# Kernel tuning notes

Hardware: AMD Instinct MI355X
Metric: run time of the kernel (lower is better)

The kernel has to match this reference:

```python
import jax, jax.numpy as jnp
import numpy as np

B, S, E = 4, 2048, 2048
H = 16
DH = 2048 // H  # head dim = 128


def setup_inputs() -> dict:
    key = jax.random.key(0)
    k0, k1, k2, k3 = jax.random.split(key, 4)
    scale = 1.0 / np.sqrt(E)
    embedded = jax.random.normal(k0, (B, S, E), dtype=jnp.float32)
    # stacked per-head projection weights, bias-free Linear: y = x @ W^T -> store as [H, E, DH]
    Wq = jax.random.normal(k1, (H, E, DH), dtype=jnp.float32) * scale
    Wk = jax.random.normal(k2, (H, E, DH), dtype=jnp.float32) * scale
    Wv = jax.random.normal(k3, (H, E, DH), dtype=jnp.float32) * scale
    return {"embedded": embedded, "Wq": Wq, "Wk": Wk, "Wv": Wv}


def reference(embedded, Wq, Wk, Wv):
    # batched over heads instead of the original python loop (same math)
    q = jnp.einsum("bse,hed->bhsd", embedded, Wq)
    k = jnp.einsum("bse,hed->bhsd", embedded, Wk)
    v = jnp.einsum("bse,hed->bhsd", embedded, Wv)
    scores = jnp.einsum("bhsd,bhtd->bhst", q, k) / jnp.sqrt(jnp.float32(DH))
    causal = jnp.tril(jnp.ones((S, S), dtype=bool))  # [S, S]
    scores = jnp.where(causal, scores, -jnp.inf)
    probs = jax.nn.softmax(scores, axis=-1)
    out = jnp.einsum("bhst,bhtd->bhsd", probs, v)
    cated = out.transpose(0, 2, 1, 3).reshape(B, S, H * DH)  # concat heads on dim=2
    return jnp.round(cated, 4)
```

## Files before the change

kernel.cpp:

```cpp
#include <hip/hip_runtime.h>

typedef float   f32x4 __attribute__((ext_vector_type(4)));
typedef _Float16 half8 __attribute__((ext_vector_type(8)));
typedef _Float16 half4 __attribute__((ext_vector_type(4)));

#define B_  4
#define S_  2048
#define E_  2048
#define H_  16
#define DH_ 128

__device__ __forceinline__ void gld16(const void* g, void* l) {
  __builtin_amdgcn_global_load_lds((const void __attribute__((address_space(1)))*)g,
                                   (void __attribute__((address_space(3)))*)l, 16, 0, 0);
}

__global__ __launch_bounds__(256) void k_cvt(const float* __restrict__ in,
                                             _Float16* __restrict__ out) {
  size_t i = ((size_t)blockIdx.x * 256 + threadIdx.x) * 8;
  float4 a = *(const float4*)(in + i);
  float4 b = *(const float4*)(in + i + 4);
  half8 h;
  h[0]=(_Float16)a.x; h[1]=(_Float16)a.y; h[2]=(_Float16)a.z; h[3]=(_Float16)a.w;
  h[4]=(_Float16)b.x; h[5]=(_Float16)b.y; h[6]=(_Float16)b.z; h[7]=(_Float16)b.w;
  *(half8*)(out + i) = h;
}

__global__ __launch_bounds__(256) void k_wt(const float* __restrict__ Wq, const float* __restrict__ Wk,
                                            const float* __restrict__ Wv, _Float16* __restrict__ Wqt,
                                            _Float16* __restrict__ Wkt, _Float16* __restrict__ Wvt) {
  __shared__ float t[32][33];
  int p = blockIdx.z >> 4, h = blockIdx.z & 15;
  const float* W  = (p==0) ? Wq  : (p==1) ? Wk  : Wv;
  _Float16*    Wt = (p==0) ? Wqt : (p==1) ? Wkt : Wvt;
  int e0 = blockIdx.x * 32, d0 = blockIdx.y * 32;
  int tx = threadIdx.x, ty = threadIdx.y;
  for (int i=0;i<4;i++)
    t[ty+8*i][tx] = W[((size_t)h*E_ + (e0+ty+8*i))*DH_ + d0+tx];
  __syncthreads();
  for (int i=0;i<4;i++)
    Wt[((size_t)h*DH_ + (d0+ty+8*i))*E_ + e0+tx] = (_Float16)t[tx][ty+8*i];
}

#define NT 32

__global__ __launch_bounds__(512, 2) void k_gemm(const _Float16* __restrict__ X,
    const _Float16* __restrict__ Wq, const _Float16* __restrict__ Wk, const _Float16* __restrict__ Wv,
    _Float16* __restrict__ Qo, _Float16* __restrict__ Ko, _Float16* __restrict__ Vt)
{
  __shared__ __align__(16) _Float16 pool[65536];

  const int z = blockIdx.z;
  const _Float16* Wp = (z==0) ? Wq : (z==1) ? Wk : Wv;

  const int fi  = blockIdx.x + (blockIdx.y << 5);
  const int lbx = fi >> 3, lby = fi & 7;
  const int m0 = lbx << 8, n0 = lby << 8;

  const int tid = threadIdx.x;
  const int wid = tid >> 6, lane = tid & 63, quad = lane >> 4, lcol = lane & 15;
  const int wm = wid >> 2, wn = wid & 3;

  int soff[2]; int slds[2];
  #pragma unroll
  for (int r=0;r<2;r++){
    int chunk = wid*128 + r*64 + lane;
    int row = chunk >> 3, cl = chunk & 7, cg = cl ^ (row & 7);
    soff[r] = row*E_ + cg*8;
    slds[r] = (wid*128 + r*64) * 16;
  }

  const _Float16* Ag = X  + (size_t)m0 * E_;
  const _Float16* Bg = Wp + (size_t)n0 * E_;

  auto stageA = [&](int mh, int tt, int buf){
    const _Float16* s = Ag + mh*(128*E_) + tt*64;
    char* l = (char*)pool + (buf*4096 + mh*1024)*16;
    #pragma unroll
    for (int r=0;r<2;r++) gld16(s + soff[r], l + slds[r]);
  };
  auto stageB = [&](int nh, int tt, int buf){
    const _Float16* s = Bg + nh*(128*E_) + tt*64;
    char* l = (char*)pool + (buf*4096 + (2+nh)*1024)*16;
    #pragma unroll
    for (int r=0;r<2;r++) gld16(s + soff[r], l + slds[r]);
  };

  half8 a[2][4], b[2][2];
  f32x4 acc[2][2][4][2] = {};

  auto rdA = [&](int mh, int buf){
    const _Float16* base = pool + (buf*4096 + mh*1024)*8;
    #pragma unroll
    for (int kk=0;kk<2;kk++)
      #pragma unroll
      for (int mi=0;mi<4;mi++){
        int R = wm*64 + mi*16 + lcol;
        int c = (kk*4 + quad) ^ (R & 7);
        a[kk][mi] = *(const half8*)(base + R*64 + c*8);
      }
  };
  auto rdB = [&](int nh, int buf){
    const _Float16* base = pool + (buf*4096 + (2+nh)*1024)*8;
    #pragma unroll
    for (int kk=0;kk<2;kk++)
      #pragma unroll
      for (int ni=0;ni<2;ni++){
        int R = wn*32 + ni*16 + lcol;
        int c = (kk*4 + quad) ^ (R & 7);
        b[kk][ni] = *(const half8*)(base + R*64 + c*8);
      }
  };
  auto mm = [&](f32x4 (&ac)[4][2]){
    #pragma unroll
    for (int kk=0;kk<2;kk++)
      #pragma unroll
      for (int mi=0;mi<4;mi++)
        #pragma unroll
        for (int ni=0;ni<2;ni++)
          ac[mi][ni] = __builtin_amdgcn_mfma_f32_16x16x32_f16(a[kk][mi], b[kk][ni], ac[mi][ni], 0, 0, 0);
  };

  stageA(0,0,0); stageB(0,0,0); stageA(1,0,0); stageB(1,0,0);
  stageA(0,1,1); stageB(1,1,1); stageA(1,1,1);
  asm volatile("s_waitcnt vmcnt(6)" ::: "memory");
  __builtin_amdgcn_s_barrier();

#define MFMA_OPEN() do{ __builtin_amdgcn_s_barrier(); \
    asm volatile("s_waitcnt lgkmcnt(0)" ::: "memory"); \
    __builtin_amdgcn_sched_barrier(0); \
    __builtin_amdgcn_s_setprio(1); }while(0)
#define MFMA_CLOSE() do{ __builtin_amdgcn_s_setprio(0); \
    __builtin_amdgcn_s_barrier(); }while(0)

#define TILE(T, BUF) do{ \
    rdA(0, BUF); rdB(0, BUF); \
    if ((T)+1 < NT) stageB(0, (T)+1, (BUF)^1); \
    MFMA_OPEN(); mm(acc[0][0]); MFMA_CLOSE(); \
    rdB(1, BUF); \
    if ((T)+2 < NT) stageA(0, (T)+2, BUF); \
    MFMA_OPEN(); mm(acc[0][1]); MFMA_CLOSE(); \
    rdA(1, BUF); \
    if ((T)+2 < NT) stageB(1, (T)+2, BUF); \
    MFMA_OPEN(); mm(acc[1][1]); MFMA_CLOSE(); \
    rdB(0, BUF); \
    if ((T)+2 < NT) stageA(1, (T)+2, BUF); \
    __builtin_amdgcn_s_barrier(); \
    asm volatile("s_waitcnt lgkmcnt(0)" ::: "memory"); \
    __builtin_amdgcn_sched_barrier(0); \
    __builtin_amdgcn_s_setprio(1); \
    mm(acc[1][0]); \
    __builtin_amdgcn_s_setprio(0); \
    if ((T) < NT-2)       { asm volatile("s_waitcnt vmcnt(6)" ::: "memory"); } \
    else if ((T) == NT-2) { asm volatile("s_waitcnt vmcnt(0)" ::: "memory"); } \
    __builtin_amdgcn_s_barrier(); \
  }while(0)

  for (int t = 0; t < NT; t += 2){
    TILE(t,   0);
    TILE(t+1, 1);
  }
#undef TILE
#undef MFMA_OPEN
#undef MFMA_CLOSE

  const int bb = m0 >> 11;
  const int s0 = m0 & 2047;
  const int h0 = n0 >> 7;
  if (z < 2){
    _Float16* O = z ? Ko : Qo;
    #pragma unroll
    for (int mh=0; mh<2; mh++)
      #pragma unroll
      for (int nh=0; nh<2; nh++)
        #pragma unroll
        for (int mi=0; mi<4; mi++)
          #pragma unroll
          for (int ni=0; ni<2; ni++){
            const int srow = s0 + mh*128 + wm*64 + mi*16 + quad*4;
            const int d = wn*32 + ni*16 + lcol;
            _Float16* p = O + (((size_t)bb*H_ + (h0+nh))*S_ + srow)*DH_ + d;
            const f32x4 v = acc[mh][nh][mi][ni];
            p[0]=(_Float16)v[0]; p[DH_]=(_Float16)v[1]; p[2*DH_]=(_Float16)v[2]; p[3*DH_]=(_Float16)v[3];
          }
  } else {
    #pragma unroll
    for (int mh=0; mh<2; mh++)
      #pragma unroll
      for (int nh=0; nh<2; nh++)
        #pragma unroll
        for (int mi=0; mi<4; mi++)
          #pragma unroll
          for (int ni=0; ni<2; ni++){
            const int scol = s0 + mh*128 + wm*64 + mi*16 + quad*4;
            const int d = wn*32 + ni*16 + lcol;
            const f32x4 u = acc[mh][nh][mi][ni];
            half4 v;
            v[0]=(_Float16)u[0]; v[1]=(_Float16)u[1]; v[2]=(_Float16)u[2]; v[3]=(_Float16)u[3];
            *(half4*)(Vt + (((size_t)bb*H_ + (h0+nh))*DH_ + d)*S_ + scol) = v;
          }
  }
}

__global__ __launch_bounds__(512, 2) void k_attn(const _Float16* __restrict__ Q,
    const _Float16* __restrict__ K, const _Float16* __restrict__ Vt, float* __restrict__ out)
{
  __shared__ __align__(16) _Float16 Ks[2][8192], Vs[2][8192];

  const int b = blockIdx.z, h = blockIdx.y;
  const int q0 = (gridDim.x - 1 - blockIdx.x) * 256;
  const int tid = threadIdx.x, wid = tid >> 6, lane = tid & 63, quad = lane >> 4, lcol = lane & 15;
  const size_t bh = (size_t)b*H_ + h;
  const _Float16* Qg = Q  + (bh*S_ + q0)*DH_;
  const _Float16* Kg = K  + bh*S_*DH_;
  const _Float16* Vg = Vt + bh*DH_*S_;

  int krow[2], kcg[2], vdr[2], vcg[2];
  for (int r=0;r<2;r++){
    int chunk = wid*128 + r*64 + lane;
    krow[r] = chunk >> 4;
    kcg[r]  = (chunk & 15) ^ (krow[r] & 15);
    vdr[r]  = chunk >> 3;
    vcg[r]  = (chunk & 7) ^ (vdr[r] & 7);
  }

  half8 qf[2][4];
  for (int g=0; g<2; g++)
    for (int kk=0; kk<4; kk++)
      qf[g][kk] = *(const half8*)(Qg + (size_t)(wid*32 + g*16 + lcol)*DH_ + kk*32 + quad*8);

  for (int r=0;r<2;r++){
    gld16(Kg + (size_t)krow[r]*DH_ + kcg[r]*8, (char*)Ks[0] + wid*2048 + r*1024 + lane*16);
    gld16(Vg + (size_t)vdr[r]*S_ + 0 + vcg[r]*8, (char*)Vs[0] + wid*2048 + r*1024 + lane*16);
  }

  f32x4 oaccT[2][8] = {};
  f32x4 lacc[2] = {};
  const half4 ones = {(_Float16)1.f,(_Float16)1.f,(_Float16)1.f,(_Float16)1.f};
  const float c1 = 0.12751879526654326f;
  const float c2 = -11.541560327111707f;
  const int rbase = q0 + wid*32;
  const int nt = (q0 >> 6) + 4;

  for (int t = 0; t < nt; t++) {
    const int buf = t & 1;
    const _Float16* ksb = Ks[buf];
    const _Float16* vsb = Vs[buf];
    const int j0 = t << 6;
    const bool live0 = (j0 <= rbase + 15);
    const bool live1 = (j0 <= rbase + 31);
    __syncthreads();

    f32x4 sa[2][4] = {};
    if (live0){
      for (int kk=0; kk<4; kk++){
        int cl = (kk*4 + quad) ^ lcol;
        for (int jb=0; jb<4; jb++){
          half8 kf = *(const half8*)(ksb + (size_t)(jb*16 + lcol)*DH_ + cl*8);
          sa[0][jb] = __builtin_amdgcn_mfma_f32_16x16x32_f16(kf, qf[0][kk], sa[0][jb], 0, 0, 0);
          sa[1][jb] = __builtin_amdgcn_mfma_f32_16x16x32_f16(kf, qf[1][kk], sa[1][jb], 0, 0, 0);
        }
      }
    } else if (live1){
      for (int kk=0; kk<4; kk++){
        int cl = (kk*4 + quad) ^ lcol;
        for (int jb=0; jb<4; jb++){
          half8 kf = *(const half8*)(ksb + (size_t)(jb*16 + lcol)*DH_ + cl*8);
          sa[1][jb] = __builtin_amdgcn_mfma_f32_16x16x32_f16(kf, qf[1][kk], sa[1][jb], 0, 0, 0);
        }
      }
    }

    if (t+1 < nt){
      const int j1 = (t+1) << 6;
      for (int r=0;r<2;r++){
        gld16(Kg + (size_t)(j1+krow[r])*DH_ + kcg[r]*8, (char*)Ks[buf^1] + wid*2048 + r*1024 + lane*16);
        gld16(Vg + (size_t)vdr[r]*S_ + j1 + vcg[r]*8,   (char*)Vs[buf^1] + wid*2048 + r*1024 + lane*16);
      }
    }

    if (live1){
      half4 pb[2][4];
      auto sm = [&](f32x4 (&s4)[4], half4 (&p4)[4], int rb){
        if (j0 + 63 > rb){
          for (int jb=0; jb<4; jb++)
            for (int rg=0; rg<4; rg++){
              int j = jb*16 + quad*4 + rg;
              float p = (j0 + j > rb + lcol) ? 0.f
                      : __builtin_amdgcn_exp2f(fmaf(s4[jb][rg], c1, c2));
              p4[jb][rg] = (_Float16)p;
            }
        } else {
          for (int jb=0; jb<4; jb++)
            for (int rg=0; rg<4; rg++)
              p4[jb][rg] = (_Float16)__builtin_amdgcn_exp2f(fmaf(s4[jb][rg], c1, c2));
        }
      };

      if (live0){
        sm(sa[0], pb[0], rbase);
        sm(sa[1], pb[1], rbase + 16);
        for (int jb=0; jb<4; jb++){
          lacc[0] = __builtin_amdgcn_mfma_f32_16x16x16f16(ones, pb[0][jb], lacc[0], 0, 0, 0);
          lacc[1] = __builtin_amdgcn_mfma_f32_16x16x16f16(ones, pb[1][jb], lacc[1], 0, 0, 0);
        }
        for (int dblk=0; dblk<8; dblk++){
          const _Float16* vrow = vsb + (size_t)(dblk*16 + lcol)*64;
          for (int jb=0; jb<4; jb++){
            int cl = (2*jb + (quad>>1)) ^ (lcol & 7);
            half4 va = *(const half4*)(vrow + cl*8 + (quad&1)*4);
            oaccT[0][dblk] = __builtin_amdgcn_mfma_f32_16x16x16f16(va, pb[0][jb], oaccT[0][dblk], 0, 0, 0);
            oaccT[1][dblk] = __builtin_amdgcn_mfma_f32_16x16x16f16(va, pb[1][jb], oaccT[1][dblk], 0, 0, 0);
          }
        }
      } else {
        sm(sa[1], pb[1], rbase + 16);
        for (int jb=0; jb<4; jb++)
          lacc[1] = __builtin_amdgcn_mfma_f32_16x16x16f16(ones, pb[1][jb], lacc[1], 0, 0, 0);
        for (int dblk=0; dblk<8; dblk++){
          const _Float16* vrow = vsb + (size_t)(dblk*16 + lcol)*64;
          for (int jb=0; jb<4; jb++){
            int cl = (2*jb + (quad>>1)) ^ (lcol & 7);
            half4 va = *(const half4*)(vrow + cl*8 + (quad&1)*4);
            oaccT[1][dblk] = __builtin_amdgcn_mfma_f32_16x16x16f16(va, pb[1][jb], oaccT[1][dblk], 0, 0, 0);
          }
        }
      }
    }
  }

  for (int g=0; g<2; g++){
    const float rinv = 1.f / lacc[g][0];
    const int s = q0 + wid*32 + g*16 + lcol;
    float* op = out + ((size_t)b*S_ + s)*(H_*DH_) + h*DH_ + quad*4;
    for (int dblk=0; dblk<8; dblk++){
      float4 v;
      v.x = oaccT[g][dblk][0]*rinv; v.y = oaccT[g][dblk][1]*rinv;
      v.z = oaccT[g][dblk][2]*rinv; v.w = oaccT[g][dblk][3]*rinv;
      *(float4*)(op + dblk*16) = v;
    }
  }
}

extern "C" void kernel_launch(void* const* d_in, const int* in_sizes, int n_in,
                              void* d_out, int out_size, void* d_ws, size_t ws_size,
                              hipStream_t stream) {
  const float* X  = (const float*)d_in[0];
  const float* Wq = (const float*)d_in[1];
  const float* Wk = (const float*)d_in[2];
  const float* Wv = (const float*)d_in[3];
  float* out = (float*)d_out;

  _Float16* Xh  = (_Float16*)d_ws;
  _Float16* Wqt = Xh  + (size_t)B_*S_*E_;
  _Float16* Wkt = Wqt + (size_t)H_*E_*DH_;
  _Float16* Wvt = Wkt + (size_t)H_*E_*DH_;
  _Float16* Qh  = Wvt + (size_t)H_*E_*DH_;
  _Float16* Kh  = Qh  + (size_t)B_*H_*S_*DH_;
  _Float16* Vth = Kh  + (size_t)B_*H_*S_*DH_;

  k_cvt <<<8192, 256, 0, stream>>>(X, Xh);
  k_wt  <<<dim3(E_/32, DH_/32, 3*H_), dim3(32,8), 0, stream>>>(Wq, Wk, Wv, Wqt, Wkt, Wvt);
  k_gemm<<<dim3(32, 8, 3), 512, 0, stream>>>(Xh, Wqt, Wkt, Wvt, Qh, Kh, Vth);
  k_attn<<<dim3(S_/256, H_, B_), 512, 0, stream>>>(Qh, Kh, Vth, out);
}
```

Measured before the change: 493.5 us.

## Double attention KV tile to 128 keys and remap GEMM blocks per XCD

```diff
diff --git a/kernel.cpp b/kernel.cpp
--- a/kernel.cpp
+++ b/kernel.cpp
@@ -54,7 +54,9 @@
   const _Float16* Wp = (z==0) ? Wq : (z==1) ? Wk : Wv;
 
   const int fi  = blockIdx.x + (blockIdx.y << 5);
-  const int lbx = fi >> 3, lby = fi & 7;
+  const int xcd = fi & 7, kk_ = fi >> 3;
+  const int lbx = ((xcd >> 1) << 3) | (kk_ & 7);
+  const int lby = ((xcd & 1) << 2) | (kk_ >> 3);
   const int m0 = lbx << 8, n0 = lby << 8;
 
   const int tid = threadIdx.x;
@@ -205,7 +207,7 @@
 __global__ __launch_bounds__(512, 2) void k_attn(const _Float16* __restrict__ Q,
     const _Float16* __restrict__ K, const _Float16* __restrict__ Vt, float* __restrict__ out)
 {
-  __shared__ __align__(16) _Float16 Ks[2][8192], Vs[2][8192];
+  __shared__ __align__(16) _Float16 Ks[2][16384], Vs[2][16384];
 
   const int b = blockIdx.z, h = blockIdx.y;
   const int q0 = (gridDim.x - 1 - blockIdx.x) * 256;
@@ -215,13 +217,11 @@
   const _Float16* Kg = K  + bh*S_*DH_;
   const _Float16* Vg = Vt + bh*DH_*S_;
 
-  int krow[2], kcg[2], vdr[2], vcg[2];
-  for (int r=0;r<2;r++){
-    int chunk = wid*128 + r*64 + lane;
-    krow[r] = chunk >> 4;
-    kcg[r]  = (chunk & 15) ^ (krow[r] & 15);
-    vdr[r]  = chunk >> 3;
-    vcg[r]  = (chunk & 7) ^ (vdr[r] & 7);
+  int srow[4], scg[4];
+  for (int r=0;r<4;r++){
+    int chunk = wid*256 + r*64 + lane;
+    srow[r] = chunk >> 4;
+    scg[r]  = (chunk & 15) ^ (srow[r] & 15);
   }
 
   half8 qf[2][4];
@@ -229,9 +229,9 @@
     for (int kk=0; kk<4; kk++)
       qf[g][kk] = *(const half8*)(Qg + (size_t)(wid*32 + g*16 + lcol)*DH_ + kk*32 + quad*8);
 
-  for (int r=0;r<2;r++){
-    gld16(Kg + (size_t)krow[r]*DH_ + kcg[r]*8, (char*)Ks[0] + wid*2048 + r*1024 + lane*16);
-    gld16(Vg + (size_t)vdr[r]*S_ + 0 + vcg[r]*8, (char*)Vs[0] + wid*2048 + r*1024 + lane*16);
+  for (int r=0;r<4;r++){
+    gld16(Kg + (size_t)srow[r]*DH_ + scg[r]*8, (char*)Ks[0] + wid*4096 + r*1024 + lane*16);
+    gld16(Vg + (size_t)srow[r]*S_  + scg[r]*8, (char*)Vs[0] + wid*4096 + r*1024 + lane*16);
   }
 
   f32x4 oaccT[2][8] = {};
@@ -240,46 +240,49 @@
   const float c1 = 0.12751879526654326f;
   const float c2 = -11.541560327111707f;
   const int rbase = q0 + wid*32;
-  const int nt = (q0 >> 6) + 4;
+  const int nt = (q0 >> 7) + 2;
 
   for (int t = 0; t < nt; t++) {
     const int buf = t & 1;
-    const _Float16* ksb = Ks[buf];
-    const _Float16* vsb = Vs[buf];
-    const int j0 = t << 6;
-    const bool live0 = (j0 <= rbase + 15);
-    const bool live1 = (j0 <= rbase + 31);
     __syncthreads();
 
-    f32x4 sa[2][4] = {};
-    if (live0){
-      for (int kk=0; kk<4; kk++){
-        int cl = (kk*4 + quad) ^ lcol;
-        for (int jb=0; jb<4; jb++){
-          half8 kf = *(const half8*)(ksb + (size_t)(jb*16 + lcol)*DH_ + cl*8);
-          sa[0][jb] = __builtin_amdgcn_mfma_f32_16x16x32_f16(kf, qf[0][kk], sa[0][jb], 0, 0, 0);
-          sa[1][jb] = __builtin_amdgcn_mfma_f32_16x16x32_f16(kf, qf[1][kk], sa[1][jb], 0, 0, 0);
-        }
-      }
-    } else if (live1){
-      for (int kk=0; kk<4; kk++){
-        int cl = (kk*4 + quad) ^ lcol;
-        for (int jb=0; jb<4; jb++){
-          half8 kf = *(const half8*)(ksb + (size_t)(jb*16 + lcol)*DH_ + cl*8);
-          sa[1][jb] = __builtin_amdgcn_mfma_f32_16x16x32_f16(kf, qf[1][kk], sa[1][jb], 0, 0, 0);
-        }
+    if (t+1 < nt){
+      const int j1 = (t+1) << 7;
+      for (int r=0;r<4;r++){
+        gld16(Kg + (size_t)(j1+srow[r])*DH_ + scg[r]*8, (char*)Ks[buf^1] + wid*4096 + r*1024 + lane*16);
+        gld16(Vg + (size_t)srow[r]*S_ + j1 + scg[r]*8,  (char*)Vs[buf^1] + wid*4096 + r*1024 + lane*16);
       }
     }
 
-    if (t+1 < nt){
-      const int j1 = (t+1) << 6;
-      for (int r=0;r<2;r++){
-        gld16(Kg + (size_t)(j1+krow[r])*DH_ + kcg[r]*8, (char*)Ks[buf^1] + wid*2048 + r*1024 + lane*16);
-        gld16(Vg + (size_t)vdr[r]*S_ + j1 + vcg[r]*8,   (char*)Vs[buf^1] + wid*2048 + r*1024 + lane*16);
-      }
-    }
-
-    if (live1){
+    #pragma unroll
+    for (int u=0; u<2; u++){
+      const int j0 = (t << 7) + (u << 6);
+      const _Float16* ksb = Ks[buf] + (u << 6)*128;
+      const _Float16* vsb = Vs[buf];
+      const bool live0 = (j0 <= rbase + 15);
+      const bool live1 = (j0 <= rbase + 31);
+      if (!live1) continue;
+
+      f32x4 sa[2][4] = {};
+      if (live0){
+        for (int kk=0; kk<4; kk++){
+          int cl = (kk*4 + quad) ^ lcol;
+          for (int jb=0; jb<4; jb++){
+            half8 kf = *(const half8*)(ksb + (size_t)(jb*16 + lcol)*128 + cl*8);
+            sa[0][jb] = __builtin_amdgcn_mfma_f32_16x16x32_f16(kf, qf[0][kk], sa[0][jb], 0, 0, 0);
+            sa[1][jb] = __builtin_amdgcn_mfma_f32_16x16x32_f16(kf, qf[1][kk], sa[1][jb], 0, 0, 0);
+          }
+        }
+      } else {
+        for (int kk=0; kk<4; kk++){
+          int cl = (kk*4 + quad) ^ lcol;
+          for (int jb=0; jb<4; jb++){
+            half8 kf = *(const half8*)(ksb + (size_t)(jb*16 + lcol)*128 + cl*8);
+            sa[1][jb] = __builtin_amdgcn_mfma_f32_16x16x32_f16(kf, qf[1][kk], sa[1][jb], 0, 0, 0);
+          }
+        }
+      }
+
       half4 pb[2][4];
       auto sm = [&](f32x4 (&s4)[4], half4 (&p4)[4], int rb){
         if (j0 + 63 > rb){
@@ -305,9 +308,9 @@
           lacc[1] = __builtin_amdgcn_mfma_f32_16x16x16f16(ones, pb[1][jb], lacc[1], 0, 0, 0);
         }
         for (int dblk=0; dblk<8; dblk++){
-          const _Float16* vrow = vsb + (size_t)(dblk*16 + lcol)*64;
+          const _Float16* vrow = vsb + (size_t)(dblk*16 + lcol)*128;
           for (int jb=0; jb<4; jb++){
-            int cl = (2*jb + (quad>>1)) ^ (lcol & 7);
+            int cl = (u*8 + 2*jb + (quad>>1)) ^ lcol;
             half4 va = *(const half4*)(vrow + cl*8 + (quad&1)*4);
             oaccT[0][dblk] = __builtin_amdgcn_mfma_f32_16x16x16f16(va, pb[0][jb], oaccT[0][dblk], 0, 0, 0);
             oaccT[1][dblk] = __builtin_amdgcn_mfma_f32_16x16x16f16(va, pb[1][jb], oaccT[1][dblk], 0, 0, 0);
@@ -318,9 +321,9 @@
         for (int jb=0; jb<4; jb++)
           lacc[1] = __builtin_amdgcn_mfma_f32_16x16x16f16(ones, pb[1][jb], lacc[1], 0, 0, 0);
         for (int dblk=0; dblk<8; dblk++){
-          const _Float16* vrow = vsb + (size_t)(dblk*16 + lcol)*64;
+          const _Float16* vrow = vsb + (size_t)(dblk*16 + lcol)*128;
           for (int jb=0; jb<4; jb++){
-            int cl = (2*jb + (quad>>1)) ^ (lcol & 7);
+            int cl = (u*8 + 2*jb + (quad>>1)) ^ lcol;
             half4 va = *(const half4*)(vrow + cl*8 + (quad&1)*4);
             oaccT[1][dblk] = __builtin_amdgcn_mfma_f32_16x16x16f16(va, pb[1][jb], oaccT[1][dblk], 0, 0, 0);
           }
```

Measured after the change: 493.0 us. No clear change (-0.1%).
